# Kernel tuning notes

Measured on AMD Instinct MI355X. Metric: run time of the kernel, lower is better.

Reference implementation:

```python
import jax, jax.numpy as jnp
import numpy as np

SIGMA = 2.0
# cv2.GaussianBlur with ksize=(0,0) on float images: ksize = round(sigma*4*2+1) | 1 = 17
KSIZE = 17
R = KSIZE // 2


def _gauss_kernel_1d():
    # matches cv2.getGaussianKernel(17, 2): exp(-(i-c)^2/(2*sigma^2)), normalized
    x = jnp.arange(KSIZE, dtype=jnp.float32) - (KSIZE - 1) / 2.0
    g = jnp.exp(-(x * x) / (2.0 * SIGMA * SIGMA))
    return g / g.sum()


def setup_inputs() -> dict:
    key = jax.random.key(0)
    # watermarked images in [-1, 1], NCHW
    noised_image = jax.random.uniform(key, (32, 3, 512, 512), jnp.float32, -1.0, 1.0)
    return {"noised_image": noised_image}


def _blur(img):
    # img: [B, C, H, W]; separable depthwise Gaussian conv, reflect_101 border
    # (cv2 BORDER_DEFAULT == jnp.pad mode='reflect')
    C = img.shape[1]
    k = _gauss_kernel_1d()
    p = jnp.pad(img, ((0, 0), (0, 0), (R, R), (R, R)), mode='reflect')
    kh = jnp.broadcast_to(k.reshape(1, 1, KSIZE, 1), (C, 1, KSIZE, 1))
    kw = jnp.broadcast_to(k.reshape(1, 1, 1, KSIZE), (C, 1, 1, KSIZE))
    dn = ('NCHW', 'OIHW', 'NCHW')
    y = jax.lax.conv_general_dilated(p, kh, (1, 1), 'VALID',
                                     dimension_numbers=dn, feature_group_count=C)
    y = jax.lax.conv_general_dilated(y, kw, (1, 1), 'VALID',
                                     dimension_numbers=dn, feature_group_count=C)
    return y


def reference(noised_image):
    # faithful to the original arithmetic:
    # [-1,1] -> [0,255], Gaussian blur, then (2*y - 1)/255
    scaled = (noised_image + 1.0) / 2.0 * 255.0
    blurred = _blur(scaled)
    return (2.0 * blurred - 1.0) / 255.0
```

## Files before the change

kernel.cpp:

```cpp
#include <hip/hip_runtime.h>
#include <math.h>

#define TILE 64
#define RAD  8
#define IW   (TILE + 2*RAD)
#define IW4  (IW/4)
#define HST  68
#define KS   17
#define IMG  512

struct GaussW { float w[KS]; };

__device__ __forceinline__ int reflect101(int g) {
    return g < 0 ? -g : (g >= IMG ? 2 * IMG - 2 - g : g);
}

__global__ __launch_bounds__(256, 6) void GaussianBlur_38963943309988_kernel(
    const float* __restrict__ in, float* __restrict__ out, GaussW gw)
{
    __shared__ __align__(16) float s_u[IW * IW];

    const int tx  = blockIdx.x;
    const int ty  = blockIdx.y;
    const int img = blockIdx.z;
    const float* __restrict__ src = in  + (size_t)img * IMG * IMG;
    float* __restrict__       dst = out + (size_t)img * IMG * IMG;
    const int x0 = tx * TILE - RAD;
    const int y0 = ty * TILE - RAD;
    const int t  = threadIdx.x;

    for (int idx = t; idx < IW * IW4; idx += 256) {
        const int row = idx / IW4;
        const int c4  = idx - row * IW4;
        const int gy  = reflect101(y0 + row);
        const int gx0 = x0 + 4 * c4;
        const float* rowp = src + (size_t)gy * IMG;
        float4 v;
        if (gx0 >= 0 && gx0 <= IMG - 4) {
            v = *reinterpret_cast<const float4*>(rowp + gx0);
        } else {
            v.x = rowp[reflect101(gx0 + 0)];
            v.y = rowp[reflect101(gx0 + 1)];
            v.z = rowp[reflect101(gx0 + 2)];
            v.w = rowp[reflect101(gx0 + 3)];
        }
        float4 r;
        r.x = (v.x + 1.0f) * 127.5f;
        r.y = (v.y + 1.0f) * 127.5f;
        r.z = (v.z + 1.0f) * 127.5f;
        r.w = (v.w + 1.0f) * 127.5f;
        *reinterpret_cast<float4*>(&s_u[4 * idx]) = r;
    }
    __syncthreads();

    const int tc = t & 15;
    const int tr = t >> 4;
    float4 hreg[5];
    #pragma unroll
    for (int rr = 0; rr < 5; ++rr) {
        const int row = tr + rr * 16;
        const float* rp = &s_u[row * IW + 4 * tc];
        float win[20];
        #pragma unroll
        for (int j = 0; j < 5; ++j) {
            const float4 v = *reinterpret_cast<const float4*>(rp + 4 * j);
            win[4*j+0] = v.x; win[4*j+1] = v.y; win[4*j+2] = v.z; win[4*j+3] = v.w;
        }
        float4 acc = {0.f, 0.f, 0.f, 0.f};
        #pragma unroll
        for (int k = 0; k < KS; ++k) {
            const float w = gw.w[k];
            acc.x += w * win[k+0];
            acc.y += w * win[k+1];
            acc.z += w * win[k+2];
            acc.w += w * win[k+3];
        }
        hreg[rr] = acc;
    }
    __syncthreads();

    #pragma unroll
    for (int rr = 0; rr < 5; ++rr) {
        const int row = tr + rr * 16;
        *reinterpret_cast<float4*>(&s_u[row * HST + 4 * tc]) = hreg[rr];
    }
    __syncthreads();

    {
        float4 acc[4];
        #pragma unroll
        for (int rj = 0; rj < 4; ++rj) acc[rj] = make_float4(0.f, 0.f, 0.f, 0.f);
        #pragma unroll
        for (int k = 0; k < 20; ++k) {
            const float4 v = *reinterpret_cast<const float4*>(&s_u[(4 * tr + k) * HST + 4 * tc]);
            #pragma unroll
            for (int rj = 0; rj < 4; ++rj) {
                if (k - rj >= 0 && k - rj < KS) {
                    const float w = gw.w[k - rj];
                    acc[rj].x += w * v.x;
                    acc[rj].y += w * v.y;
                    acc[rj].z += w * v.z;
                    acc[rj].w += w * v.w;
                }
            }
        }
        const int ox = tx * TILE + 4 * tc;
        #pragma unroll
        for (int rj = 0; rj < 4; ++rj) {
            const int oy = ty * TILE + 4 * tr + rj;
            float4 o;
            o.x = acc[rj].x * (2.0f/255.0f) - (1.0f/255.0f);
            o.y = acc[rj].y * (2.0f/255.0f) - (1.0f/255.0f);
            o.z = acc[rj].z * (2.0f/255.0f) - (1.0f/255.0f);
            o.w = acc[rj].w * (2.0f/255.0f) - (1.0f/255.0f);
            *reinterpret_cast<float4*>(dst + (size_t)oy * IMG + ox) = o;
        }
    }
}

extern "C" void kernel_launch(void* const* d_in, const int* in_sizes, int n_in,
                              void* d_out, int out_size, void* d_ws, size_t ws_size,
                              hipStream_t stream) {
    const float* in = (const float*)d_in[0];
    float* out = (float*)d_out;

    GaussW gw;
    double g[KS], s = 0.0;
    for (int i = 0; i < KS; ++i) {
        const double d = i - (KS - 1) / 2.0;
        g[i] = exp(-(d * d) / 8.0);
        s += g[i];
    }
    for (int i = 0; i < KS; ++i) gw.w[i] = (float)(g[i] / s);

    const int nimg = in_sizes[0] / (IMG * IMG);
    dim3 grid(IMG / TILE, IMG / TILE, nimg);
    dim3 block(256);
    hipLaunchKernelGGL(GaussianBlur_38963943309988_kernel, grid, block, 0, stream,
                       in, out, gw);
}
```

Baseline: 195.1 us.

## Widen per-thread register windows in both blur passes to cut LDS reads

The horizontal pass now gives each of 160 threads a 48-float window covering 32 outputs of one row, so neighbouring outputs reuse more loaded values and shared-memory reads per output drop. The vertical pass uses 128 threads that each compute 8 output rows from a 24-row window instead of 4 rows from 20. The row stride is padded to 84 floats to limit bank conflicts. In exchange, 96 to 128 of the 256 threads idle in the compute phases, and the larger register arrays may push up register pressure and lower occupancy.

```diff
diff --git a/kernel.cpp b/kernel.cpp
--- a/kernel.cpp
+++ b/kernel.cpp
@@ -3,9 +3,8 @@
 
 #define TILE 64
 #define RAD  8
-#define IW   (TILE + 2*RAD)
-#define IW4  (IW/4)
-#define HST  68
+#define IW   80
+#define RST  84
 #define KS   17
 #define IMG  512
 
@@ -18,7 +17,7 @@
 __global__ __launch_bounds__(256, 6) void GaussianBlur_38963943309988_kernel(
     const float* __restrict__ in, float* __restrict__ out, GaussW gw)
 {
-    __shared__ __align__(16) float s_u[IW * IW];
+    __shared__ __align__(16) float s_u[RST * IW];
 
     const int tx  = blockIdx.x;
     const int ty  = blockIdx.y;
@@ -29,9 +28,9 @@
     const int y0 = ty * TILE - RAD;
     const int t  = threadIdx.x;
 
-    for (int idx = t; idx < IW * IW4; idx += 256) {
-        const int row = idx / IW4;
-        const int c4  = idx - row * IW4;
+    for (int idx = t; idx < IW * (IW/4); idx += 256) {
+        const int row = idx / (IW/4);
+        const int c4  = idx - row * (IW/4);
         const int gy  = reflect101(y0 + row);
         const int gx0 = x0 + 4 * c4;
         const float* rowp = src + (size_t)gy * IMG;
@@ -49,70 +48,69 @@
         r.y = (v.y + 1.0f) * 127.5f;
         r.z = (v.z + 1.0f) * 127.5f;
         r.w = (v.w + 1.0f) * 127.5f;
-        *reinterpret_cast<float4*>(&s_u[4 * idx]) = r;
+        *reinterpret_cast<float4*>(&s_u[row * RST + 4 * c4]) = r;
     }
     __syncthreads();
 
-    const int tc = t & 15;
-    const int tr = t >> 4;
-    float4 hreg[5];
-    #pragma unroll
-    for (int rr = 0; rr < 5; ++rr) {
-        const int row = tr + rr * 16;
-        const float* rp = &s_u[row * IW + 4 * tc];
-        float win[20];
+    const int p2row = t % 80;
+    const int p2seg = t / 80;
+    float win[48];
+    if (t < 160) {
+        const float* rp = &s_u[p2row * RST + 32 * p2seg];
         #pragma unroll
-        for (int j = 0; j < 5; ++j) {
+        for (int j = 0; j < 12; ++j) {
             const float4 v = *reinterpret_cast<const float4*>(rp + 4 * j);
             win[4*j+0] = v.x; win[4*j+1] = v.y; win[4*j+2] = v.z; win[4*j+3] = v.w;
         }
-        float4 acc = {0.f, 0.f, 0.f, 0.f};
-        #pragma unroll
-        for (int k = 0; k < KS; ++k) {
-            const float w = gw.w[k];
-            acc.x += w * win[k+0];
-            acc.y += w * win[k+1];
-            acc.z += w * win[k+2];
-            acc.w += w * win[k+3];
-        }
-        hreg[rr] = acc;
     }
     __syncthreads();
 
-    #pragma unroll
-    for (int rr = 0; rr < 5; ++rr) {
-        const int row = tr + rr * 16;
-        *reinterpret_cast<float4*>(&s_u[row * HST + 4 * tc]) = hreg[rr];
+    if (t < 160) {
+        #pragma unroll
+        for (int j = 0; j < 8; ++j) {
+            float4 o = {0.f, 0.f, 0.f, 0.f};
+            #pragma unroll
+            for (int k = 0; k < KS; ++k) {
+                const float w = gw.w[k];
+                o.x += w * win[4*j + k + 0];
+                o.y += w * win[4*j + k + 1];
+                o.z += w * win[4*j + k + 2];
+                o.w += w * win[4*j + k + 3];
+            }
+            *reinterpret_cast<float4*>(&s_u[p2row * RST + 32 * p2seg + 4 * j]) = o;
+        }
     }
     __syncthreads();
 
-    {
-        float4 acc[4];
+    if (t < 128) {
+        const int c = t & 15;
+        const int g = t >> 4;
+        float4 acc[8];
         #pragma unroll
-        for (int rj = 0; rj < 4; ++rj) acc[rj] = make_float4(0.f, 0.f, 0.f, 0.f);
+        for (int r = 0; r < 8; ++r) acc[r] = make_float4(0.f, 0.f, 0.f, 0.f);
         #pragma unroll
-        for (int k = 0; k < 20; ++k) {
-            const float4 v = *reinterpret_cast<const float4*>(&s_u[(4 * tr + k) * HST + 4 * tc]);
+        for (int k = 0; k < 24; ++k) {
+            const float4 v = *reinterpret_cast<const float4*>(&s_u[(8*g + k) * RST + 4*c]);
             #pragma unroll
-            for (int rj = 0; rj < 4; ++rj) {
-                if (k - rj >= 0 && k - rj < KS) {
-                    const float w = gw.w[k - rj];
-                    acc[rj].x += w * v.x;
-                    acc[rj].y += w * v.y;
-                    acc[rj].z += w * v.z;
-                    acc[rj].w += w * v.w;
+            for (int r = 0; r < 8; ++r) {
+                if (k - r >= 0 && k - r < KS) {
+                    const float w = gw.w[k - r];
+                    acc[r].x += w * v.x;
+                    acc[r].y += w * v.y;
+                    acc[r].z += w * v.z;
+                    acc[r].w += w * v.w;
                 }
             }
         }
-        const int ox = tx * TILE + 4 * tc;
+        const int ox = tx * TILE + 4 * c;
         #pragma unroll
-        for (int rj = 0; rj < 4; ++rj) {
-            const int oy = ty * TILE + 4 * tr + rj;
+        for (int r = 0; r < 8; ++r) {
+            const int oy = ty * TILE + 8 * g + r;
             float4 o;
-            o.x = acc[rj].x * (2.0f/255.0f) - (1.0f/255.0f);
-            o.y = acc[rj].y * (2.0f/255.0f) - (1.0f/255.0f);
-            o.z = acc[rj].z * (2.0f/255.0f) - (1.0f/255.0f);
-            o.w = acc[rj].w * (2.0f/255.0f) - (1.0f/255.0f);
+            o.x = acc[r].x * (2.0f/255.0f) - (1.0f/255.0f);
+            o.y = acc[r].y * (2.0f/255.0f) - (1.0f/255.0f);
+            o.z = acc[r].z * (2.0f/255.0f) - (1.0f/255.0f);
+            o.w = acc[r].w * (2.0f/255.0f) - (1.0f/255.0f);
             *reinterpret_cast<float4*>(dst + (size_t)oy * IMG + ox) = o;
         }
     }
```

Result: faster. 189.5 us (-2.9%).
